# Performance work log

Measured on AMD Instinct MI355X. Metric: run time of the kernel, lower is better.

Reference implementation:

```python
import jax, jax.numpy as jnp
import numpy as np

K = 4          # torus_dim (circles)
M = 6          # n_modes
GRID = 12      # grid_size for Laplacian eigenvalues
T = 2.0        # uniformity temperature
SPREAD_W = 1.0
B = 8192       # batch size


def _karmonic_weights():
    # lambda_n = 2 - 2 cos(2 pi n / N), n = 1..M; w = (lam - lam1)/(lam_max - lam1)
    n = np.arange(1, M + 1)
    lam = 2.0 - 2.0 * np.cos(2.0 * np.pi * n / GRID)
    w = (lam - lam[0]) / (lam.max() - lam[0])
    return jnp.asarray(w, dtype=jnp.float32)


def setup_inputs() -> dict:
    key = jax.random.key(0)
    k1, k2 = jax.random.split(key)
    angles = jax.random.normal(k1, (B, K), dtype=jnp.float32)
    fourier_embed = jax.random.normal(k2, (B, 2 * K * M), dtype=jnp.float32)
    return {"angles": angles, "fourier_embed": fourier_embed}


def reference(angles, fourier_embed):
    Bn = fourier_embed.shape[0]
    w = _karmonic_weights()
    # group by mode: (B, M, 2K)
    x = fourier_embed.reshape(Bn, M, 2 * K)
    eye = jnp.eye(Bn, dtype=bool)
    log_Bm1 = jnp.log(jnp.float32(Bn - 1))

    total_unif = jnp.float32(0.0)
    mode_unifs = []
    for n in range(M):  # fixed small structural loop over modes
        xn = x[:, n, :]                                   # (B, 2K)
        sq = jnp.sum(xn * xn, axis=1)                     # (B,)
        d2 = sq[:, None] + sq[None, :] - 2.0 * (xn @ xn.T)
        d2 = jnp.maximum(d2, 0.0)                         # cdist(...)**2, clamped >= 0
        neg = jnp.where(eye, -jnp.inf, -T * d2)           # exclude diagonal like masked_select
        unif_n = jnp.mean(jax.nn.logsumexp(neg, axis=1)) - log_Bm1
        mode_unifs.append(unif_n)
        total_unif = total_unif + w[n] * unif_n

    # circular decorrelation (spread) across circle pairs, vectorized over pairs
    mu = jnp.arctan2(jnp.mean(jnp.sin(angles), axis=0),
                     jnp.mean(jnp.cos(angles), axis=0))   # (K,) circular means
    s = jnp.sin(angles - mu[None, :])                     # (B, K)
    cov = (s.T @ s) / jnp.float32(Bn)                     # (K, K) = mean(s_i * s_j)
    var = jnp.diagonal(cov)                               # mean(s_i^2)
    den = jnp.sqrt(var[:, None] * var[None, :] + 1e-8)
    corr2 = (cov / den) ** 2
    iu = np.triu_indices(K, 1)                            # upper-triangle pairs i<j
    spread = jnp.mean(corr2[iu])

    total = total_unif + jnp.float32(SPREAD_W) * spread
    return total_unif, spread, total, jnp.stack(mode_unifs)
```

## Files before the change

### kernel.cpp

```cpp
#include <hip/hip_runtime.h>
#include <math.h>

constexpr int BN = 8192;
constexpr int MN = 6;

constexpr float TL    = 2.8853900817779268f;
constexpr float SCL_Z = 2.4022448795936154f;

typedef __bf16 bf16_t;
typedef bf16_t bf16x8 __attribute__((ext_vector_type(8)));
typedef float f32x4 __attribute__((ext_vector_type(4)));

union PK { bf16_t h[8]; uint4 u; };

__device__ __forceinline__ bf16x8 frag_of(uint4 u) {
    return __builtin_bit_cast(bf16x8, u);
}

__device__ __host__ __forceinline__ int midx(int a, int b) {
    return 8 * a - (a * (a - 1)) / 2 + (b - a);
}

__global__ __launch_bounds__(256) void prep_ang(const float* __restrict__ x,
                                                const float* __restrict__ ang,
                                                uint4* __restrict__ Ap,
                                                uint4* __restrict__ Bp,
                                                float* __restrict__ angp) {
    const int blk = blockIdx.x;
    const int tid = threadIdx.x;
    if (blk < 192) {
        int idx = blk * 256 + tid;
        int n = idx >> 13;
        int j = idx & (BN - 1);
        const float* p = x + (size_t)j * 48 + n * 8;

        PK zh, zl, a3, b3;
        float sq = 0.f;
#pragma unroll
        for (int k = 0; k < 8; ++k) {
            float v = p[k];
            sq = fmaf(v, v, sq);
            float z = SCL_Z * v;
            bf16_t h = (bf16_t)z;
            zh.h[k] = h;
            zl.h[k] = (bf16_t)(z - (float)h);
        }
        float s = -TL * sq;
        bf16_t sh = (bf16_t)s;
        bf16_t sl = (bf16_t)(s - (float)sh);
        bf16_t one = (bf16_t)1.0f, zero = (bf16_t)0.0f;
        a3.h[0] = one; a3.h[1] = one; a3.h[2] = sh;  a3.h[3] = sl;
        b3.h[0] = sh;  b3.h[1] = sl;  b3.h[2] = one; b3.h[3] = one;
#pragma unroll
        for (int k = 4; k < 8; ++k) { a3.h[k] = zero; b3.h[k] = zero; }

        size_t base = ((size_t)(n * 512 + (j >> 4))) * 64 + (j & 15);
        Ap[base +  0] = zh.u;
        Ap[base + 16] = zl.u;
        Ap[base + 32] = zh.u;
        Ap[base + 48] = a3.u;
        Bp[base +  0] = zh.u;
        Bp[base + 16] = zh.u;
        Bp[base + 32] = zl.u;
        Bp[base + 48] = b3.u;
    } else {
        const int i = (blk - 192) * 256 + tid;
        float v[8];
#pragma unroll
        for (int k = 0; k < 4; ++k) __sincosf(ang[i * 4 + k], &v[k], &v[4 + k]);
        float acc[44];
        int c = 0;
#pragma unroll
        for (int a = 0; a < 8; ++a)
#pragma unroll
            for (int bq = a; bq < 8; ++bq) acc[c++] = v[a] * v[bq];
#pragma unroll
        for (int a = 0; a < 8; ++a) acc[36 + a] = v[a];

#pragma unroll
        for (int q = 0; q < 44; ++q) {
            float s = acc[q];
            s += __shfl_xor(s, 1);  s += __shfl_xor(s, 2);
            s += __shfl_xor(s, 4);  s += __shfl_xor(s, 8);
            s += __shfl_xor(s, 16); s += __shfl_xor(s, 32);
            acc[q] = s;
        }
        __shared__ float sm[4][44];
        const int w = tid >> 6, lane = tid & 63;
        if (lane == 0)
#pragma unroll
            for (int q = 0; q < 44; ++q) sm[w][q] = acc[q];
        __syncthreads();
        if (tid < 44)
            angp[(blk - 192) * 44 + tid] =
                sm[0][tid] + sm[1][tid] + sm[2][tid] + sm[3][tid];
    }
}

__global__ __launch_bounds__(512, 8) void pair_mfma(const uint4* __restrict__ Ap,
                                                    const uint4* __restrict__ Bp,
                                                    float* __restrict__ Sh) {
    const int tid  = threadIdx.x;
    const int lane = tid & 63;
    const int w    = __builtin_amdgcn_readfirstlane(tid >> 6);
    const int b    = blockIdx.x;
    const int n    = b >> 8;
    const int rb   = (b >> 1) & 127;
    const int h    = b & 1;
    const int rb4  = rb * 4;

    bf16x8 af[4];
#pragma unroll
    for (int t = 0; t < 4; ++t)
        af[t] = frag_of(Ap[((size_t)(n * 512 + rb4 + t)) * 64 + lane]);

    float racc[16];
#pragma unroll
    for (int q = 0; q < 16; ++q) racc[q] = 0.f;

    const uint4* bbase = Bp + ((size_t)n * 512) * 64 + lane;
    const f32x4 z4 = {0.f, 0.f, 0.f, 0.f};

    const int jt0 = h * 256 + w * 32, jt1 = jt0 + 32;
    uint4 b0 = bbase[(size_t)jt0 * 64];
    uint4 b1 = bbase[(size_t)(jt0 + 1) * 64];
    for (int jt = jt0; jt < jt1; jt += 2) {
        uint4 p0 = bbase[(size_t)(jt + 2) * 64];
        uint4 p1 = bbase[(size_t)(jt + 3) * 64];

        bf16x8 bf = frag_of(b0);
#pragma unroll
        for (int t = 0; t < 4; ++t) {
            f32x4 d = __builtin_amdgcn_mfma_f32_16x16x32_bf16(af[t], bf, z4, 0, 0, 0);
#pragma unroll
            for (int r = 0; r < 4; ++r)
                racc[t * 4 + r] += __builtin_amdgcn_exp2f(d[r]);
        }
        bf = frag_of(b1);
#pragma unroll
        for (int t = 0; t < 4; ++t) {
            f32x4 d = __builtin_amdgcn_mfma_f32_16x16x32_bf16(af[t], bf, z4, 0, 0, 0);
#pragma unroll
            for (int r = 0; r < 4; ++r)
                racc[t * 4 + r] += __builtin_amdgcn_exp2f(d[r]);
        }
        b0 = p0; b1 = p1;
    }

    if ((rb4 >> 8) == h && ((rb4 >> 5) & 7) == w) {
        const int dd = (lane & 15) - 4 * (lane >> 4);
#pragma unroll
        for (int t = 0; t < 4; ++t) {
            bf16x8 bf = frag_of(bbase[(size_t)(rb4 + t) * 64]);
            f32x4 d = __builtin_amdgcn_mfma_f32_16x16x32_bf16(af[t], bf, z4, 0, 0, 0);
#pragma unroll
            for (int r = 0; r < 4; ++r)
                if (dd == r) racc[t * 4 + r] -= __builtin_amdgcn_exp2f(d[r]);
        }
    }

#pragma unroll
    for (int q = 0; q < 16; ++q) {
        float v = racc[q];
        v += __shfl_xor(v, 1);
        v += __shfl_xor(v, 2);
        v += __shfl_xor(v, 4);
        v += __shfl_xor(v, 8);
        racc[q] = v;
    }

    __shared__ float smem[8][64];
    if ((lane & 15) == 0) {
        int g = lane >> 4;
#pragma unroll
        for (int t = 0; t < 4; ++t)
#pragma unroll
            for (int r = 0; r < 4; ++r)
                smem[w][t * 16 + g * 4 + r] = racc[t * 4 + r];
    }
    __syncthreads();

    if (tid < 64) {
        float s = 0.f;
#pragma unroll
        for (int ww = 0; ww < 8; ++ww) s += smem[ww][tid];
        Sh[h * (MN * BN) + n * BN + rb * 64 + tid] = s;
    }
}

__global__ __launch_bounds__(512) void log_red(const float* __restrict__ Sh,
                                               float* __restrict__ lp) {
    const int tid = threadIdx.x;
    const int idx = blockIdx.x * 512 + tid;
    float v = Sh[idx] + Sh[idx + MN * BN];
    float lg = logf(v);
    lg += __shfl_xor(lg, 1);
    lg += __shfl_xor(lg, 2);
    lg += __shfl_xor(lg, 4);
    lg += __shfl_xor(lg, 8);
    lg += __shfl_xor(lg, 16);
    lg += __shfl_xor(lg, 32);
    __shared__ float sm[8];
    if ((tid & 63) == 0) sm[tid >> 6] = lg;
    __syncthreads();
    if (tid == 0) {
        float s = 0.f;
#pragma unroll
        for (int i = 0; i < 8; ++i) s += sm[i];
        lp[blockIdx.x] = s;
    }
}

__global__ __launch_bounds__(64) void final_asm(const float* __restrict__ angp,
                                                const float* __restrict__ lp,
                                                float* __restrict__ out) {
    const int tid = threadIdx.x;
    __shared__ float mom[44];

    if (tid < 44) {
        float s = 0.f;
        for (int bk = 0; bk < 32; ++bk) s += angp[bk * 44 + tid];
        mom[tid] = s;
    }
    __syncthreads();

    if (tid == 0) {
        float sm[4], cm[4];
#pragma unroll
        for (int k = 0; k < 4; ++k) {
            float S = mom[36 + k], C = mom[40 + k];
            float hyp = sqrtf(S * S + C * C);
            sm[k] = S / hyp;
            cm[k] = C / hyp;
        }
        auto COV = [&](int k, int l) -> float {
            int ks = k < l ? k : l, kl = k < l ? l : k;
            float mss = mom[midx(ks, kl)];
            float msc_kl = mom[midx(k, l + 4)];
            float msc_lk = mom[midx(l, k + 4)];
            float mcc = mom[midx(ks + 4, kl + 4)];
            return (cm[k] * cm[l] * mss - cm[k] * sm[l] * msc_kl -
                    sm[k] * cm[l] * msc_lk + sm[k] * sm[l] * mcc) *
                   (1.0f / (float)BN);
        };
        float var[4] = {COV(0, 0), COV(1, 1), COV(2, 2), COV(3, 3)};
        float spread = 0.f;
        const int pk[6] = {0, 0, 0, 1, 1, 2};
        const int pl[6] = {1, 2, 3, 2, 3, 3};
#pragma unroll
        for (int p = 0; p < 6; ++p) {
            float cv = COV(pk[p], pl[p]);
            float den = sqrtf(var[pk[p]] * var[pl[p]] + 1e-8f);
            float cr = cv / den;
            spread += cr * cr;
        }
        spread *= (1.0f / 6.0f);

        const float wgt[6] = {0.0f, 0.19615242270663188f, 0.4641016151377544f,
                              0.7320508075688773f, 0.9282032302755088f, 1.0f};
        const float logBm1 = logf((float)(BN - 1));
        float total_unif = 0.f, unif[6];
#pragma unroll
        for (int m = 0; m < 6; ++m) {
            float s = 0.f;
            for (int i = 0; i < 16; ++i) s += lp[m * 16 + i];
            unif[m] = s * (1.0f / (float)BN) - logBm1;
            total_unif += wgt[m] * unif[m];
        }
        out[0] = total_unif;
        out[1] = spread;
        out[2] = total_unif + spread;
#pragma unroll
        for (int m = 0; m < 6; ++m) out[3 + m] = unif[m];
    }
}

extern "C" void kernel_launch(void* const* d_in, const int* in_sizes, int n_in,
                              void* d_out, int out_size, void* d_ws, size_t ws_size,
                              hipStream_t stream) {
    const float* angles  = (const float*)d_in[0];
    const float* fourier = (const float*)d_in[1];
    float* out = (float*)d_out;

    char* ws = (char*)d_ws;
    uint4* Bp   = (uint4*)(ws + 0);
    uint4* Ap   = (uint4*)(ws + 3145728);
    float* Sh   = (float*)(ws + 6291456);
    float* lp   = (float*)(ws + 6684672);
    float* angp = (float*)(ws + 6685056);

    prep_ang<<<dim3(224), dim3(256), 0, stream>>>(fourier, angles, Ap, Bp, angp);
    pair_mfma<<<dim3(1536), dim3(512), 0, stream>>>(Ap, Bp, Sh);
    log_red<<<dim3(96), dim3(512), 0, stream>>>(Sh, lp);
    final_asm<<<dim3(1), dim3(64), 0, stream>>>(angp, lp, out);
}
```

Before: 61.16 us.

## Split pair kernel into independent per-wave work units with 32-way column partials

The pairwise MFMA kernel is restructured so each wave handles three independent units of (mode, row block, 16-tile column chunk). The block-wide shared-memory reduction and __syncthreads are gone, and each wave writes its own partial row sums into 32 column-slice buffers. log_red then sums the 32 partials before taking the log. This removes intra-block synchronization and evens out load, but the partial buffer grows 16x and log_red does more global reads. The shared-memory write and read inside a wave has no barrier, so it relies on wave-level ordering.

```diff
diff --git a/kernel.cpp b/kernel.cpp
--- a/kernel.cpp
+++ b/kernel.cpp
@@ -97,94 +97,93 @@
     }
 }
 
-__global__ __launch_bounds__(512, 8) void pair_mfma(const uint4* __restrict__ Ap,
+__global__ __launch_bounds__(256, 8) void pair_mfma(const uint4* __restrict__ Ap,
                                                     const uint4* __restrict__ Bp,
                                                     float* __restrict__ Sh) {
     const int tid  = threadIdx.x;
     const int lane = tid & 63;
-    const int w    = __builtin_amdgcn_readfirstlane(tid >> 6);
-    const int b    = blockIdx.x;
-    const int n    = b >> 8;
-    const int rb   = (b >> 1) & 127;
-    const int h    = b & 1;
-    const int rb4  = rb * 4;
-
-    bf16x8 af[4];
-#pragma unroll
-    for (int t = 0; t < 4; ++t)
-        af[t] = frag_of(Ap[((size_t)(n * 512 + rb4 + t)) * 64 + lane]);
-
-    float racc[16];
-#pragma unroll
-    for (int q = 0; q < 16; ++q) racc[q] = 0.f;
-
-    const uint4* bbase = Bp + ((size_t)n * 512) * 64 + lane;
+    const int wloc = tid >> 6;
+    const int gw   = __builtin_amdgcn_readfirstlane((blockIdx.x * 256 + tid) >> 6);
+
+    __shared__ float smem[4][64];
     const f32x4 z4 = {0.f, 0.f, 0.f, 0.f};
 
-    const int jt0 = h * 256 + w * 32, jt1 = jt0 + 32;
-    uint4 b0 = bbase[(size_t)jt0 * 64];
-    uint4 b1 = bbase[(size_t)(jt0 + 1) * 64];
-    for (int jt = jt0; jt < jt1; jt += 2) {
-        uint4 p0 = bbase[(size_t)(jt + 2) * 64];
-        uint4 p1 = bbase[(size_t)(jt + 3) * 64];
-
-        bf16x8 bf = frag_of(b0);
-#pragma unroll
-        for (int t = 0; t < 4; ++t) {
-            f32x4 d = __builtin_amdgcn_mfma_f32_16x16x32_bf16(af[t], bf, z4, 0, 0, 0);
-#pragma unroll
-            for (int r = 0; r < 4; ++r)
-                racc[t * 4 + r] += __builtin_amdgcn_exp2f(d[r]);
-        }
-        bf = frag_of(b1);
-#pragma unroll
-        for (int t = 0; t < 4; ++t) {
-            f32x4 d = __builtin_amdgcn_mfma_f32_16x16x32_bf16(af[t], bf, z4, 0, 0, 0);
-#pragma unroll
-            for (int r = 0; r < 4; ++r)
-                racc[t * 4 + r] += __builtin_amdgcn_exp2f(d[r]);
-        }
-        b0 = p0; b1 = p1;
-    }
-
-    if ((rb4 >> 8) == h && ((rb4 >> 5) & 7) == w) {
-        const int dd = (lane & 15) - 4 * (lane >> 4);
-#pragma unroll
-        for (int t = 0; t < 4; ++t) {
-            bf16x8 bf = frag_of(bbase[(size_t)(rb4 + t) * 64]);
-            f32x4 d = __builtin_amdgcn_mfma_f32_16x16x32_bf16(af[t], bf, z4, 0, 0, 0);
-#pragma unroll
-            for (int r = 0; r < 4; ++r)
-                if (dd == r) racc[t * 4 + r] -= __builtin_amdgcn_exp2f(d[r]);
-        }
-    }
-
-#pragma unroll
-    for (int q = 0; q < 16; ++q) {
-        float v = racc[q];
-        v += __shfl_xor(v, 1);
-        v += __shfl_xor(v, 2);
-        v += __shfl_xor(v, 4);
-        v += __shfl_xor(v, 8);
-        racc[q] = v;
-    }
-
-    __shared__ float smem[8][64];
-    if ((lane & 15) == 0) {
-        int g = lane >> 4;
+    for (int k = 0; k < 3; ++k) {
+        const int u   = gw * 3 + k;
+        const int n   = u >> 12;
+        const int rb  = (u >> 5) & 127;
+        const int c   = u & 31;
+        const int rb4 = rb * 4;
+
+        bf16x8 af[4];
 #pragma unroll
         for (int t = 0; t < 4; ++t)
-#pragma unroll
-            for (int r = 0; r < 4; ++r)
-                smem[w][t * 16 + g * 4 + r] = racc[t * 4 + r];
-    }
-    __syncthreads();
-
-    if (tid < 64) {
-        float s = 0.f;
-#pragma unroll
-        for (int ww = 0; ww < 8; ++ww) s += smem[ww][tid];
-        Sh[h * (MN * BN) + n * BN + rb * 64 + tid] = s;
+            af[t] = frag_of(Ap[((size_t)(n * 512 + rb4 + t)) * 64 + lane]);
+
+        float racc[16];
+#pragma unroll
+        for (int q = 0; q < 16; ++q) racc[q] = 0.f;
+
+        const uint4* bbase = Bp + ((size_t)n * 512) * 64 + lane;
+        const int jt0 = c * 16;
+
+        uint4 b0 = bbase[(size_t)jt0 * 64];
+        uint4 b1 = bbase[(size_t)(jt0 + 1) * 64];
+        for (int jt = jt0; jt < jt0 + 16; jt += 2) {
+            uint4 p0 = bbase[(size_t)(jt + 2) * 64];
+            uint4 p1 = bbase[(size_t)(jt + 3) * 64];
+
+            bf16x8 bf = frag_of(b0);
+#pragma unroll
+            for (int t = 0; t < 4; ++t) {
+                f32x4 d = __builtin_amdgcn_mfma_f32_16x16x32_bf16(af[t], bf, z4, 0, 0, 0);
+#pragma unroll
+                for (int r = 0; r < 4; ++r)
+                    racc[t * 4 + r] += __builtin_amdgcn_exp2f(d[r]);
+            }
+            bf = frag_of(b1);
+#pragma unroll
+            for (int t = 0; t < 4; ++t) {
+                f32x4 d = __builtin_amdgcn_mfma_f32_16x16x32_bf16(af[t], bf, z4, 0, 0, 0);
+#pragma unroll
+                for (int r = 0; r < 4; ++r)
+                    racc[t * 4 + r] += __builtin_amdgcn_exp2f(d[r]);
+            }
+            b0 = p0; b1 = p1;
+        }
+
+        if (c == (rb >> 2)) {
+            const int dd = (lane & 15) - 4 * (lane >> 4);
+#pragma unroll
+            for (int t = 0; t < 4; ++t) {
+                bf16x8 bf = frag_of(bbase[(size_t)(rb4 + t) * 64]);
+                f32x4 d = __builtin_amdgcn_mfma_f32_16x16x32_bf16(af[t], bf, z4, 0, 0, 0);
+#pragma unroll
+                for (int r = 0; r < 4; ++r)
+                    if (dd == r) racc[t * 4 + r] -= __builtin_amdgcn_exp2f(d[r]);
+            }
+        }
+
+#pragma unroll
+        for (int q = 0; q < 16; ++q) {
+            float v = racc[q];
+            v += __shfl_xor(v, 1);
+            v += __shfl_xor(v, 2);
+            v += __shfl_xor(v, 4);
+            v += __shfl_xor(v, 8);
+            racc[q] = v;
+        }
+
+        if ((lane & 15) == 0) {
+            int g = lane >> 4;
+#pragma unroll
+            for (int t = 0; t < 4; ++t)
+#pragma unroll
+                for (int r = 0; r < 4; ++r)
+                    smem[wloc][t * 16 + g * 4 + r] = racc[t * 4 + r];
+        }
+        float val = smem[wloc][lane];
+        Sh[(size_t)c * (MN * BN) + n * BN + rb * 64 + lane] = val;
     }
 }
 
@@ -192,7 +191,9 @@
                                                float* __restrict__ lp) {
     const int tid = threadIdx.x;
     const int idx = blockIdx.x * 512 + tid;
-    float v = Sh[idx] + Sh[idx + MN * BN];
+    float v = 0.f;
+#pragma unroll
+    for (int c = 0; c < 32; ++c) v += Sh[(size_t)c * (MN * BN) + idx];
     float lg = logf(v);
     lg += __shfl_xor(lg, 1);
     lg += __shfl_xor(lg, 2);
@@ -286,11 +287,11 @@
     uint4* Bp   = (uint4*)(ws + 0);
     uint4* Ap   = (uint4*)(ws + 3145728);
     float* Sh   = (float*)(ws + 6291456);
-    float* lp   = (float*)(ws + 6684672);
-    float* angp = (float*)(ws + 6685056);
+    float* lp   = (float*)(ws + 12582912);
+    float* angp = (float*)(ws + 12583296);
 
     prep_ang<<<dim3(224), dim3(256), 0, stream>>>(fourier, angles, Ap, Bp, angp);
-    pair_mfma<<<dim3(1536), dim3(512), 0, stream>>>(Ap, Bp, Sh);
+    pair_mfma<<<dim3(2048), dim3(256), 0, stream>>>(Ap, Bp, Sh);
     log_red<<<dim3(96), dim3(512), 0, stream>>>(Sh, lp);
     final_asm<<<dim3(1), dim3(64), 0, stream>>>(angp, lp, out);
 }
```

After: 69.44 us. 13.5% more time.

## Exploit symmetry of pairwise distance matrix to halve MFMA and exp work

Applied to the files above, without the earlier changes.

Restructures the pairwise kernel to compute only the upper triangle of the symmetric B×B kernel matrix per mode. Each tile's exponentials are accumulated into both row sums and, via LDS, column sums; the column partials are stored to a workspace in bf16. A separate wedge kernel handles the diagonal blocks, and log_red now merges row sums, wedge sums and 64 bf16 column partials per row. A single packed operand layout (z_hi, z_lo, a3, b3) replaces the separate A and B buffers. This roughly halves the MFMA and exp2 work, at the cost of per-tile LDS atomics-free updates, a large 32KB LDS buffer lowering occupancy, extra global traffic for partials, and bf16 rounding of column partials.

```diff
diff --git a/kernel.cpp b/kernel.cpp
--- a/kernel.cpp
+++ b/kernel.cpp
@@ -21,10 +21,10 @@
     return 8 * a - (a * (a - 1)) / 2 + (b - a);
 }
 
+
 __global__ __launch_bounds__(256) void prep_ang(const float* __restrict__ x,
                                                 const float* __restrict__ ang,
-                                                uint4* __restrict__ Ap,
-                                                uint4* __restrict__ Bp,
+                                                uint4* __restrict__ C,
                                                 float* __restrict__ angp) {
     const int blk = blockIdx.x;
     const int tid = threadIdx.x;
@@ -55,14 +55,10 @@
         for (int k = 4; k < 8; ++k) { a3.h[k] = zero; b3.h[k] = zero; }
 
         size_t base = ((size_t)(n * 512 + (j >> 4))) * 64 + (j & 15);
-        Ap[base +  0] = zh.u;
-        Ap[base + 16] = zl.u;
-        Ap[base + 32] = zh.u;
-        Ap[base + 48] = a3.u;
-        Bp[base +  0] = zh.u;
-        Bp[base + 16] = zh.u;
-        Bp[base + 32] = zl.u;
-        Bp[base + 48] = b3.u;
+        C[base +  0] = zh.u;
+        C[base + 16] = zl.u;
+        C[base + 32] = a3.u;
+        C[base + 48] = b3.u;
     } else {
         const int i = (blk - 192) * 256 + tid;
         float v[8];
@@ -97,65 +93,142 @@
     }
 }
 
-__global__ __launch_bounds__(512, 8) void pair_mfma(const uint4* __restrict__ Ap,
-                                                    const uint4* __restrict__ Bp,
-                                                    float* __restrict__ Sh) {
+__global__ __launch_bounds__(512, 6) void pair_sweep(const uint4* __restrict__ C,
+                                                     float* __restrict__ colsumP,
+                                                     unsigned short* __restrict__ credP) {
     const int tid  = threadIdx.x;
     const int lane = tid & 63;
     const int w    = __builtin_amdgcn_readfirstlane(tid >> 6);
     const int b    = blockIdx.x;
-    const int n    = b >> 8;
-    const int rb   = (b >> 1) & 127;
+    const int m    = b >> 7;
+    const int sp   = (b >> 1) & 63;
     const int h    = b & 1;
-    const int rb4  = rb * 4;
+    const int rho  = 2 * w + h;
+
+    __shared__ float cred[8192];
+    __shared__ float smem[8][64];
+    for (int q = tid; q < 8192; q += 512) cred[q] = 0.f;
+    __syncthreads();
+
+    const int g  = lane >> 4;
+    const int pa = (g == 3) ? 2 : (g & 1);
+    const int pb = (g == 3) ? 3 : (g >> 1);
+    const int cl = lane & 15;
+    const f32x4 z4 = {0.f, 0.f, 0.f, 0.f};
+    const uint4* mbase = C + (size_t)m * 512 * 64;
+    const uint4* bcol  = mbase + pb * 16 + cl;
+
+#pragma unroll 1
+    for (int sidx = 0; sidx < 2; ++sidx) {
+        const int s = sidx ? (127 - sp) : sp;
+
+        bf16x8 af[4];
+#pragma unroll
+        for (int t = 0; t < 4; ++t)
+            af[t] = frag_of(mbase[(size_t)(4 * s + t) * 64 + pa * 16 + cl]);
+
+        float racc[16];
+#pragma unroll
+        for (int q = 0; q < 16; ++q) racc[q] = 0.f;
+
+        const int start = 4 * s + 4;
+        const int first = start + (int)(((unsigned)(rho - start)) & 15u);
+        const int f0 = (first < 512) ? first : 0;
+
+        uint4 b0 = bcol[(size_t)f0 * 64];
+        uint4 b1 = bcol[(size_t)(f0 + 16) * 64];
+        for (int jt = first; jt < 512; jt += 16) {
+            uint4 p0 = bcol[(size_t)(jt + 32) * 64];
+            bf16x8 bf = frag_of(b0);
+            float rsum = 0.f;
+#pragma unroll
+            for (int t = 0; t < 4; ++t) {
+                f32x4 d = __builtin_amdgcn_mfma_f32_16x16x32_bf16(af[t], bf, z4, 0, 0, 0);
+#pragma unroll
+                for (int r = 0; r < 4; ++r) {
+                    float e = __builtin_amdgcn_exp2f(d[r]);
+                    racc[t * 4 + r] += e;
+                    rsum += e;
+                }
+            }
+            rsum += __shfl_xor(rsum, 16);
+            rsum += __shfl_xor(rsum, 32);
+            if (lane < 16) cred[jt * 16 + lane] += rsum;
+            b0 = b1; b1 = p0;
+        }
+
+#pragma unroll
+        for (int q = 0; q < 16; ++q) {
+            float v = racc[q];
+            v += __shfl_xor(v, 1);
+            v += __shfl_xor(v, 2);
+            v += __shfl_xor(v, 4);
+            v += __shfl_xor(v, 8);
+            racc[q] = v;
+        }
+        if (cl == 0) {
+#pragma unroll
+            for (int t = 0; t < 4; ++t)
+#pragma unroll
+                for (int r = 0; r < 4; ++r)
+                    smem[w][t * 16 + g * 4 + r] = racc[t * 4 + r];
+        }
+        __syncthreads();
+        if (tid < 64) {
+            float ssum = 0.f;
+#pragma unroll
+            for (int ww = 0; ww < 8; ++ww) ssum += smem[ww][tid];
+            colsumP[(size_t)h * (MN * BN) + m * BN + s * 64 + tid] = ssum;
+        }
+        __syncthreads();
+    }
+
+    for (int q = tid; q < 4096; q += 512) {
+        int jt = 2 * (q >> 4) + h, c = q & 15;
+        bf16_t v = (bf16_t)cred[jt * 16 + c];
+        credP[((size_t)((m * 64 + sp) * 2 + h)) * 4096 + q] =
+            __builtin_bit_cast(unsigned short, v);
+    }
+}
+
+__global__ __launch_bounds__(256) void wedge(const uint4* __restrict__ C,
+                                             float* __restrict__ wedgeP) {
+    const int tid  = threadIdx.x;
+    const int lane = tid & 63;
+    const int wl   = tid >> 6;
+    const int gw   = blockIdx.x * 4 + wl;
+    const int m    = gw >> 7;
+    const int s    = gw & 127;
+
+    const int g  = lane >> 4;
+    const int pa = (g == 3) ? 2 : (g & 1);
+    const int pb = (g == 3) ? 3 : (g >> 1);
+    const int cl = lane & 15;
+    const int dd = cl - 4 * g;
+    const f32x4 z4 = {0.f, 0.f, 0.f, 0.f};
+    const uint4* mbase = C + (size_t)m * 512 * 64;
 
     bf16x8 af[4];
 #pragma unroll
     for (int t = 0; t < 4; ++t)
-        af[t] = frag_of(Ap[((size_t)(n * 512 + rb4 + t)) * 64 + lane]);
+        af[t] = frag_of(mbase[(size_t)(4 * s + t) * 64 + pa * 16 + cl]);
 
     float racc[16];
 #pragma unroll
     for (int q = 0; q < 16; ++q) racc[q] = 0.f;
 
-    const uint4* bbase = Bp + ((size_t)n * 512) * 64 + lane;
-    const f32x4 z4 = {0.f, 0.f, 0.f, 0.f};
-
-    const int jt0 = h * 256 + w * 32, jt1 = jt0 + 32;
-    uint4 b0 = bbase[(size_t)jt0 * 64];
-    uint4 b1 = bbase[(size_t)(jt0 + 1) * 64];
-    for (int jt = jt0; jt < jt1; jt += 2) {
-        uint4 p0 = bbase[(size_t)(jt + 2) * 64];
-        uint4 p1 = bbase[(size_t)(jt + 3) * 64];
-
-        bf16x8 bf = frag_of(b0);
+#pragma unroll
+    for (int u = 0; u < 4; ++u) {
+        bf16x8 bf = frag_of(mbase[(size_t)(4 * s + u) * 64 + pb * 16 + cl]);
 #pragma unroll
         for (int t = 0; t < 4; ++t) {
             f32x4 d = __builtin_amdgcn_mfma_f32_16x16x32_bf16(af[t], bf, z4, 0, 0, 0);
 #pragma unroll
-            for (int r = 0; r < 4; ++r)
-                racc[t * 4 + r] += __builtin_amdgcn_exp2f(d[r]);
-        }
-        bf = frag_of(b1);
-#pragma unroll
-        for (int t = 0; t < 4; ++t) {
-            f32x4 d = __builtin_amdgcn_mfma_f32_16x16x32_bf16(af[t], bf, z4, 0, 0, 0);
-#pragma unroll
-            for (int r = 0; r < 4; ++r)
-                racc[t * 4 + r] += __builtin_amdgcn_exp2f(d[r]);
-        }
-        b0 = p0; b1 = p1;
-    }
-
-    if ((rb4 >> 8) == h && ((rb4 >> 5) & 7) == w) {
-        const int dd = (lane & 15) - 4 * (lane >> 4);
-#pragma unroll
-        for (int t = 0; t < 4; ++t) {
-            bf16x8 bf = frag_of(bbase[(size_t)(rb4 + t) * 64]);
-            f32x4 d = __builtin_amdgcn_mfma_f32_16x16x32_bf16(af[t], bf, z4, 0, 0, 0);
-#pragma unroll
-            for (int r = 0; r < 4; ++r)
-                if (dd == r) racc[t * 4 + r] -= __builtin_amdgcn_exp2f(d[r]);
+            for (int r = 0; r < 4; ++r) {
+                float e = __builtin_amdgcn_exp2f(d[r]);
+                if (u == t) e = (dd == r) ? 0.f : e;
+                racc[t * 4 + r] += e;
+            }
         }
     }
 
@@ -169,30 +242,37 @@
         racc[q] = v;
     }
 
-    __shared__ float smem[8][64];
-    if ((lane & 15) == 0) {
-        int g = lane >> 4;
+    __shared__ float smem[4][64];
+    if (cl == 0) {
 #pragma unroll
         for (int t = 0; t < 4; ++t)
 #pragma unroll
             for (int r = 0; r < 4; ++r)
-                smem[w][t * 16 + g * 4 + r] = racc[t * 4 + r];
-    }
-    __syncthreads();
-
-    if (tid < 64) {
-        float s = 0.f;
-#pragma unroll
-        for (int ww = 0; ww < 8; ++ww) s += smem[ww][tid];
-        Sh[h * (MN * BN) + n * BN + rb * 64 + tid] = s;
-    }
-}
-
-__global__ __launch_bounds__(512) void log_red(const float* __restrict__ Sh,
+                smem[wl][t * 16 + g * 4 + r] = racc[t * 4 + r];
+    }
+    float val = smem[wl][lane];
+    wedgeP[(size_t)m * BN + s * 64 + lane] = val;
+}
+
+__global__ __launch_bounds__(512) void log_red(const float* __restrict__ colsumP,
+                                               const float* __restrict__ wedgeP,
+                                               const unsigned short* __restrict__ credP,
                                                float* __restrict__ lp) {
     const int tid = threadIdx.x;
     const int idx = blockIdx.x * 512 + tid;
-    float v = Sh[idx] + Sh[idx + MN * BN];
+    const int m = idx >> 13;
+    const int i = idx & (BN - 1);
+    const int jt = i >> 4, c = i & 15;
+    const int hh = jt & 1;
+    const int q = (jt >> 1) * 16 + c;
+
+    float v = wedgeP[idx] + colsumP[idx] + colsumP[MN * BN + idx];
+    const unsigned short* base = credP + ((size_t)(m * 128 + hh)) * 4096 + q;
+#pragma unroll 8
+    for (int sp = 0; sp < 64; ++sp) {
+        unsigned short u = base[(size_t)sp * 8192];
+        v += (float)__builtin_bit_cast(bf16_t, u);
+    }
     float lg = logf(v);
     lg += __shfl_xor(lg, 1);
     lg += __shfl_xor(lg, 2);
@@ -206,7 +286,7 @@
     if (tid == 0) {
         float s = 0.f;
 #pragma unroll
-        for (int i = 0; i < 8; ++i) s += sm[i];
+        for (int k = 0; k < 8; ++k) s += sm[k];
         lp[blockIdx.x] = s;
     }
 }
@@ -228,10 +308,10 @@
         float sm[4], cm[4];
 #pragma unroll
         for (int k = 0; k < 4; ++k) {
-            float S = mom[36 + k], C = mom[40 + k];
-            float hyp = sqrtf(S * S + C * C);
+            float S = mom[36 + k], Cc = mom[40 + k];
+            float hyp = sqrtf(S * S + Cc * Cc);
             sm[k] = S / hyp;
-            cm[k] = C / hyp;
+            cm[k] = Cc / hyp;
         }
         auto COV = [&](int k, int l) -> float {
             int ks = k < l ? k : l, kl = k < l ? l : k;
@@ -261,17 +341,17 @@
         const float logBm1 = logf((float)(BN - 1));
         float total_unif = 0.f, unif[6];
 #pragma unroll
-        for (int m = 0; m < 6; ++m) {
+        for (int mm = 0; mm < 6; ++mm) {
             float s = 0.f;
-            for (int i = 0; i < 16; ++i) s += lp[m * 16 + i];
-            unif[m] = s * (1.0f / (float)BN) - logBm1;
-            total_unif += wgt[m] * unif[m];
+            for (int k = 0; k < 16; ++k) s += lp[mm * 16 + k];
+            unif[mm] = s * (1.0f / (float)BN) - logBm1;
+            total_unif += wgt[mm] * unif[mm];
         }
         out[0] = total_unif;
         out[1] = spread;
         out[2] = total_unif + spread;
 #pragma unroll
-        for (int m = 0; m < 6; ++m) out[3 + m] = unif[m];
+        for (int mm = 0; mm < 6; ++mm) out[3 + mm] = unif[mm];
     }
 }
 
@@ -283,14 +363,16 @@
     float* out = (float*)d_out;
 
     char* ws = (char*)d_ws;
-    uint4* Bp   = (uint4*)(ws + 0);
-    uint4* Ap   = (uint4*)(ws + 3145728);
-    float* Sh   = (float*)(ws + 6291456);
-    float* lp   = (float*)(ws + 6684672);
-    float* angp = (float*)(ws + 6685056);
-
-    prep_ang<<<dim3(224), dim3(256), 0, stream>>>(fourier, angles, Ap, Bp, angp);
-    pair_mfma<<<dim3(1536), dim3(512), 0, stream>>>(Ap, Bp, Sh);
-    log_red<<<dim3(96), dim3(512), 0, stream>>>(Sh, lp);
+    uint4* C              = (uint4*)(ws + 0);
+    unsigned short* credP = (unsigned short*)(ws + 3145728);
+    float* colsumP        = (float*)(ws + 9437184);
+    float* wedgeP         = (float*)(ws + 9830400);
+    float* lp             = (float*)(ws + 10027008);
+    float* angp           = (float*)(ws + 10027392);
+
+    prep_ang<<<dim3(224), dim3(256), 0, stream>>>(fourier, angles, C, angp);
+    pair_sweep<<<dim3(768), dim3(512), 0, stream>>>(C, colsumP, credP);
+    wedge<<<dim3(192), dim3(256), 0, stream>>>(C, wedgeP);
+    log_red<<<dim3(96), dim3(512), 0, stream>>>(colsumP, wedgeP, credP, lp);
     final_asm<<<dim3(1), dim3(64), 0, stream>>>(angp, lp, out);
 }
```

Result: no change. 61.36 us (+0.3%).
